# Kernel optimization log

Measured on AMD Instinct MI355X. Metric: run time of the kernel, lower is better.

Reference implementation:

```python
import jax, jax.numpy as jnp
import numpy as np

B, T, I, H, O = 1024, 512, 128, 256, 64


def setup_inputs() -> dict:
    key = jax.random.key(0)
    ks = jax.random.split(key, 12)
    def lin(k, shape, fan_in):
        return jax.random.uniform(k, shape, jnp.float32, -1.0, 1.0) / np.sqrt(fan_in)
    return {
        "x": jax.random.normal(ks[0], (B, T, I), jnp.float32),
        "h0": jnp.zeros((B, H), jnp.float32),
        # GRUCell params (gate order: r, z, n as in PyTorch)
        "W_ih": lin(ks[1], (3 * H, I), H),
        "b_ih": lin(ks[2], (3 * H,), H),
        "W_hh": lin(ks[3], (3 * H, H), H),
        "b_hh": lin(ks[4], (3 * H,), H),
        # input_transform Linear(I -> H)
        "Wt": lin(ks[5], (H, I), I),
        "bt": lin(ks[6], (H,), I),
        # output_proj Linear(H -> O)
        "Wo": lin(ks[7], (O, H), H),
        "bo": lin(ks[8], (O,), H),
        # gate_proj Linear(H -> O)
        "Wg": lin(ks[9], (O, H), H),
        "bg": lin(ks[10], (O,), H),
    }


def reference(x, h0, W_ih, b_ih, W_hh, b_hh, Wt, bt, Wo, bo, Wg, bg):
    # Precompute all input-side projections with big GEMMs (time-major for scan)
    xi = jnp.einsum("bti,gi->tbg", x, W_ih) + b_ih          # [T,B,3H]
    ti = jax.nn.silu(jnp.einsum("bti,hi->tbh", x, Wt) + bt)  # [T,B,H]

    def step(h, inp):
        xi_t, ti_t = inp
        hh = h @ W_hh.T + b_hh                               # [B,3H]
        xr, xz, xn = jnp.split(xi_t, 3, axis=-1)
        hr, hz, hn = jnp.split(hh, 3, axis=-1)
        r = jax.nn.sigmoid(xr + hr)
        z = jax.nn.sigmoid(xz + hz)
        n = jnp.tanh(xn + r * hn)
        h_new = (1.0 - z) * n + z * h
        proj = (h_new + ti_t) @ Wo.T + bo                    # [B,O]
        gate = jax.nn.sigmoid(h_new @ Wg.T + bg)             # [B,O]
        return h_new, proj * gate

    _, outs = jax.lax.scan(step, h0, (xi, ti))               # outs: [T,B,O]
    return jnp.mean(outs, axis=0)                            # [B,O]
```

## Files before the change

kernel.cpp:

```cpp
#include <hip/hip_runtime.h>
#include <hip/hip_bf16.h>


typedef __attribute__((ext_vector_type(8))) __bf16 bf16x8;
typedef __attribute__((ext_vector_type(4))) __bf16 bf16x4;
typedef __attribute__((ext_vector_type(4))) float f32x4;

#define MFMA(a, b, c) __builtin_amdgcn_mfma_f32_16x16x32_bf16(a, b, c, 0, 0, 0)

__device__ __forceinline__ float fsig(float v) {
  float e = __builtin_amdgcn_exp2f(v * -1.442695041f);
  return __builtin_amdgcn_rcpf(1.0f + e);
}
__device__ __forceinline__ float ftanh(float v) {
  float e = __builtin_amdgcn_exp2f(v * 2.885390082f);
  return 1.0f - 2.0f * __builtin_amdgcn_rcpf(1.0f + e);
}

#define O_WIN 0u
#define O_WHH 262144u
#define O_WO  655360u
#define O_WG  688128u
#define O_B1  720896u
#define O_H   724992u
#define O_ACC 1773568u
#define O_TIO 2035712u

__global__ void k1_prep(const float* __restrict__ Wih, const float* __restrict__ Wt,
                        const float* __restrict__ Whh, const float* __restrict__ Wo,
                        const float* __restrict__ Wg, const float* __restrict__ bih,
                        const float* __restrict__ bhh, const float* __restrict__ bt,
                        const float* __restrict__ h0, char* __restrict__ ws) {
  unsigned n = blockIdx.x * 256u + threadIdx.x;
  __bf16* win = (__bf16*)(ws + O_WIN);
  __bf16* whh = (__bf16*)(ws + O_WHH);
  __bf16* wo = (__bf16*)(ws + O_WO);
  __bf16* wg = (__bf16*)(ws + O_WG);
  float* b1 = (float*)(ws + O_B1);
  float* hb = (float*)(ws + O_H);
  float* ac = (float*)(ws + O_ACC);
  if (n < 98304u) win[n] = (__bf16)Wih[n];
  else if (n < 131072u) { unsigned i = n - 98304u; win[98304u + i] = (__bf16)Wt[i]; }
  else if (n < 327680u) { unsigned i = n - 131072u; whh[i] = (__bf16)Whh[i]; }
  else if (n < 344064u) { unsigned i = n - 327680u; wo[i] = (__bf16)Wo[i]; }
  else if (n < 360448u) { unsigned i = n - 344064u; wg[i] = (__bf16)Wg[i]; }
  else if (n < 361472u) {
    unsigned i = n - 360448u;
    float v = (i < 512u) ? (bih[i] + bhh[i]) : ((i < 768u) ? bih[i] : bt[i - 768u]);
    b1[i] = v;
  } else if (n < 623616u) { unsigned i = n - 361472u; hb[i] = h0[i]; }
  else if (n < 689152u) { unsigned i = n - 623616u; ac[i] = 0.0f; }
}

__global__ __launch_bounds__(256, 2) void k2_xi(
    const float* __restrict__ x, const __bf16* __restrict__ win,
    const float* __restrict__ b1, __bf16* __restrict__ xi, int t0, int tcbits) {
  extern __shared__ char sm2[];
  __bf16* Asm = (__bf16*)sm2;
  __bf16* Bsm = (__bf16*)(sm2 + 34816);
  const int tid = threadIdx.x;
  const int lane = tid & 63, wv = tid >> 6;
  const int m0 = blockIdx.x * 128;
  const int tcm = (1 << tcbits) - 1;
#pragma unroll
  for (int rnd = 0; rnd < 16; ++rnd) {
    int row = rnd * 8 + (tid >> 5);
    int cr = m0 + row;
    int bb = cr >> tcbits, tt = cr & tcm;
    const float* xr = x + ((size_t)bb * 512 + (size_t)(t0 + tt)) * 128 + (tid & 31) * 4;
    float4 v = *(const float4*)xr;
    bf16x4 b4 = {(__bf16)v.x, (__bf16)v.y, (__bf16)v.z, (__bf16)v.w};
    *(bf16x4*)&Asm[row * 136 + (tid & 31) * 4] = b4;
  }
  for (int nc = 0; nc < 6; ++nc) {
    __syncthreads();
#pragma unroll
    for (int rnd = 0; rnd < 8; ++rnd) {
      int rr = rnd * 16 + (tid >> 4);
      uint4 w4 = *(const uint4*)(win + (size_t)(nc * 128 + rr) * 128 + (tid & 15) * 8);
      *(uint4*)&Bsm[rr * 136 + (tid & 15) * 8] = w4;
    }
    __syncthreads();
    f32x4 zv = {0.f, 0.f, 0.f, 0.f};
    f32x4 acc[2][8];
#pragma unroll
    for (int mi = 0; mi < 2; ++mi)
#pragma unroll
      for (int nt = 0; nt < 8; ++nt) acc[mi][nt] = zv;
#pragma unroll
    for (int kt = 0; kt < 4; ++kt) {
      bf16x8 a0 = *(const bf16x8*)&Asm[(wv * 32 + (lane & 15)) * 136 + kt * 32 + (lane >> 4) * 8];
      bf16x8 a1 = *(const bf16x8*)&Asm[(wv * 32 + 16 + (lane & 15)) * 136 + kt * 32 + (lane >> 4) * 8];
#pragma unroll
      for (int nt = 0; nt < 8; ++nt) {
        bf16x8 b = *(const bf16x8*)&Bsm[(nt * 16 + (lane & 15)) * 136 + kt * 32 + (lane >> 4) * 8];
        acc[0][nt] = MFMA(a0, b, acc[0][nt]);
        acc[1][nt] = MFMA(a1, b, acc[1][nt]);
      }
    }
    __syncthreads();
#pragma unroll
    for (int nt = 0; nt < 8; ++nt) {
      float bv = b1[nc * 128 + nt * 16 + (lane & 15)];
#pragma unroll
      for (int mi = 0; mi < 2; ++mi)
#pragma unroll
        for (int r = 0; r < 4; ++r) {
          int rowb = wv * 32 + mi * 16 + (lane >> 4) * 4 + r;
          Bsm[rowb * 136 + nt * 16 + (lane & 15)] = (__bf16)(acc[mi][nt][r] + bv);
        }
    }
    __syncthreads();
#pragma unroll
    for (int rnd = 0; rnd < 8; ++rnd) {
      int row = rnd * 16 + (tid >> 4);
      int cr = m0 + row;
      int bb = cr >> tcbits, tt = cr & tcm;
      uint4 v = *(const uint4*)&Bsm[row * 136 + (tid & 15) * 8];
      *(uint4*)(xi + ((size_t)tt * 1024 + bb) * 768 + nc * 128 + (tid & 15) * 8) = v;
    }
  }
}

__global__ __launch_bounds__(256, 1) void k2_tio(
    const float* __restrict__ x, const __bf16* __restrict__ win,
    const __bf16* __restrict__ wo, const float* __restrict__ b1,
    const float* __restrict__ bo, __bf16* __restrict__ tio, int t0, int tcbits) {
  extern __shared__ char sm3[];
  __bf16* Asm = (__bf16*)sm3;
  __bf16* Bsm = (__bf16*)(sm3 + 34816);
  __bf16* Ti = (__bf16*)(sm3 + 69632);
  const int tid = threadIdx.x;
  const int lane = tid & 63, wv = tid >> 6;
  const int m0 = blockIdx.x * 128;
  const int tcm = (1 << tcbits) - 1;
#pragma unroll
  for (int rnd = 0; rnd < 16; ++rnd) {
    int row = rnd * 8 + (tid >> 5);
    int cr = m0 + row;
    int bb = cr >> tcbits, tt = cr & tcm;
    const float* xr = x + ((size_t)bb * 512 + (size_t)(t0 + tt)) * 128 + (tid & 31) * 4;
    float4 v = *(const float4*)xr;
    bf16x4 b4 = {(__bf16)v.x, (__bf16)v.y, (__bf16)v.z, (__bf16)v.w};
    *(bf16x4*)&Asm[row * 136 + (tid & 31) * 4] = b4;
  }
  for (int nc = 0; nc < 2; ++nc) {
    __syncthreads();
#pragma unroll
    for (int rnd = 0; rnd < 8; ++rnd) {
      int rr = rnd * 16 + (tid >> 4);
      uint4 w4 = *(const uint4*)(win + (size_t)(98304 / 128 + nc * 128 + rr) * 128 + (tid & 15) * 8);
      *(uint4*)&Bsm[rr * 136 + (tid & 15) * 8] = w4;
    }
    __syncthreads();
    f32x4 zv = {0.f, 0.f, 0.f, 0.f};
    f32x4 acc[2][8];
#pragma unroll
    for (int mi = 0; mi < 2; ++mi)
#pragma unroll
      for (int nt = 0; nt < 8; ++nt) acc[mi][nt] = zv;
#pragma unroll
    for (int kt = 0; kt < 4; ++kt) {
      bf16x8 a0 = *(const bf16x8*)&Asm[(wv * 32 + (lane & 15)) * 136 + kt * 32 + (lane >> 4) * 8];
      bf16x8 a1 = *(const bf16x8*)&Asm[(wv * 32 + 16 + (lane & 15)) * 136 + kt * 32 + (lane >> 4) * 8];
#pragma unroll
      for (int nt = 0; nt < 8; ++nt) {
        bf16x8 b = *(const bf16x8*)&Bsm[(nt * 16 + (lane & 15)) * 136 + kt * 32 + (lane >> 4) * 8];
        acc[0][nt] = MFMA(a0, b, acc[0][nt]);
        acc[1][nt] = MFMA(a1, b, acc[1][nt]);
      }
    }
#pragma unroll
    for (int nt = 0; nt < 8; ++nt) {
      float bv = b1[768 + nc * 128 + nt * 16 + (lane & 15)];
#pragma unroll
      for (int mi = 0; mi < 2; ++mi)
#pragma unroll
        for (int r = 0; r < 4; ++r) {
          int rowb = wv * 32 + mi * 16 + (lane >> 4) * 4 + r;
          float s = acc[mi][nt][r] + bv;
          s = s * __builtin_amdgcn_rcpf(1.0f + __builtin_amdgcn_exp2f(s * -1.442695041f));
          Ti[rowb * 264 + nc * 128 + nt * 16 + (lane & 15)] = (__bf16)s;
        }
    }
  }
  __syncthreads();
  for (int i = tid; i < 2048; i += 256) {
    int row = i >> 5;
    int c8 = (i & 31) * 8;
    *(uint4*)&Bsm[row * 264 + c8] = *(const uint4*)(wo + row * 256 + c8);
  }
  __syncthreads();
  f32x4 zv = {0.f, 0.f, 0.f, 0.f};
  f32x4 acc2[2][4];
#pragma unroll
  for (int mi = 0; mi < 2; ++mi)
#pragma unroll
    for (int nt = 0; nt < 4; ++nt) acc2[mi][nt] = zv;
#pragma unroll
  for (int kt = 0; kt < 8; ++kt) {
    bf16x8 a0 = *(const bf16x8*)&Ti[(wv * 32 + (lane & 15)) * 264 + kt * 32 + (lane >> 4) * 8];
    bf16x8 a1 = *(const bf16x8*)&Ti[(wv * 32 + 16 + (lane & 15)) * 264 + kt * 32 + (lane >> 4) * 8];
#pragma unroll
    for (int nt = 0; nt < 4; ++nt) {
      bf16x8 b = *(const bf16x8*)&Bsm[(nt * 16 + (lane & 15)) * 264 + kt * 32 + (lane >> 4) * 8];
      acc2[0][nt] = MFMA(a0, b, acc2[0][nt]);
      acc2[1][nt] = MFMA(a1, b, acc2[1][nt]);
    }
  }
#pragma unroll
  for (int nt = 0; nt < 4; ++nt) {
    int col = nt * 16 + (lane & 15);
    float bv = bo[col];
#pragma unroll
    for (int mi = 0; mi < 2; ++mi)
#pragma unroll
      for (int r = 0; r < 4; ++r) {
        int rowb = wv * 32 + mi * 16 + (lane >> 4) * 4 + r;
        int cr = m0 + rowb;
        int bb = cr >> tcbits, tt = cr & tcm;
        tio[((size_t)tt * 1024 + bb) * 64 + col] = (__bf16)(acc2[mi][nt][r] + bv);
      }
  }
}

__global__ __launch_bounds__(256, 1) void k3_rec(
    const __bf16* __restrict__ xi, const __bf16* __restrict__ tio,
    const __bf16* __restrict__ whh, const __bf16* __restrict__ wo,
    const __bf16* __restrict__ wg, const float* __restrict__ bhn,
    const float* __restrict__ bg, float* __restrict__ hbuf,
    float* __restrict__ accb, int TC) {
  extern __shared__ char sm[];
  __bf16* h_lds = (__bf16*)sm;
  float* pre = (float*)(sm + 8448);
  __bf16* xib = (__bf16*)(sm + 20736);
  __bf16* wow = (__bf16*)(sm + 34048);
  const int tid = threadIdx.x;
  const int lane = tid & 63, wv = tid >> 6;
  const int b0 = blockIdx.x * 4;
  const int gcp = lane * 4;

  bf16x8 wf[4][3][8];
#pragma unroll
  for (int p = 0; p < 4; ++p)
#pragma unroll
    for (int g = 0; g < 3; ++g)
#pragma unroll
      for (int kt = 0; kt < 8; ++kt) {
        int rowg = g * 256 + wv * 64 + p * 16 + (lane & 15);
        wf[p][g][kt] = *(const bf16x8*)(whh + (size_t)rowg * 256 + kt * 32 + (lane >> 4) * 8);
      }
  for (int i = tid; i < 4096; i += 256) {
    int row = i >> 5;
    int c8 = (i & 31) * 8;
    const __bf16* srcw = (row < 64) ? (wo + row * 256 + c8) : (wg + (row - 64) * 256 + c8);
    *(uint4*)&wow[row * 264 + c8] = *(const uint4*)srcw;
  }
  for (int i = tid; i < 2112; i += 256) ((unsigned*)h_lds)[i] = 0u;
  __syncthreads();
  float hreg[4];
  {
    f32x4 h4 = *(const f32x4*)(hbuf + (size_t)(b0 + wv) * 256 + gcp);
    hreg[0] = h4[0]; hreg[1] = h4[1]; hreg[2] = h4[2]; hreg[3] = h4[3];
    bf16x4 hb = {(__bf16)h4[0], (__bf16)h4[1], (__bf16)h4[2], (__bf16)h4[3]};
    *(bf16x4*)&h_lds[wv * 264 + gcp] = hb;
  }
  float bhnp[4];
#pragma unroll
  for (int p = 0; p < 4; ++p) bhnp[p] = bhn[wv * 64 + p * 16 + (lane & 15)];
  float bgv = bg[wv * 16 + (lane & 15)];
  float oacc[4] = {0.f, 0.f, 0.f, 0.f};
  if (lane < 16) {
#pragma unroll
    for (int r = 0; r < 4; ++r) oacc[r] = accb[(size_t)(b0 + r) * 64 + wv * 16 + lane];
  }
  {
    const uint2* s0 = (const uint2*)(xi + (size_t)b0 * 768);
    uint2* d0 = (uint2*)xib;
    d0[tid] = s0[tid]; d0[tid + 256] = s0[tid + 256]; d0[tid + 512] = s0[tid + 512];
    if (tid < 64) ((uint2*)(xib + 3072))[tid] = ((const uint2*)(tio + (size_t)b0 * 64))[tid];
  }
  __syncthreads();

#pragma unroll 1
  for (int t = 0; t < TC; ++t) {
    const int cur = t & 1, nxt = cur ^ 1;
    __bf16* xc = xib + cur * 3328;
    __bf16* xnb = xib + nxt * 3328;
    int tn = (t + 1 < TC) ? (t + 1) : t;
    uint2 pf0, pf1, pf2, pft;
    {
      const uint2* s = (const uint2*)(xi + ((size_t)tn * 1024 + b0) * 768);
      pf0 = s[tid]; pf1 = s[tid + 256]; pf2 = s[tid + 512];
      if (tid < 64) pft = ((const uint2*)(tio + ((size_t)tn * 1024 + b0) * 64))[tid];
    }
    bf16x8 afr[8];
#pragma unroll
    for (int kt = 0; kt < 8; ++kt)
      afr[kt] = *(const bf16x8*)&h_lds[(lane & 15) * 264 + kt * 32 + (lane >> 4) * 8];
#pragma unroll
    for (int p = 0; p < 4; ++p) {
      f32x4 ar = {0.f, 0.f, 0.f, 0.f}, az = {0.f, 0.f, 0.f, 0.f};
      f32x4 an = {bhnp[p], bhnp[p], bhnp[p], bhnp[p]};
#pragma unroll
      for (int kt = 0; kt < 8; ++kt) {
        ar = MFMA(afr[kt], wf[p][0][kt], ar);
        az = MFMA(afr[kt], wf[p][1][kt], az);
        an = MFMA(afr[kt], wf[p][2][kt], an);
      }
      if (lane < 16) {
        int col = wv * 64 + p * 16 + lane;
#pragma unroll
        for (int r = 0; r < 4; ++r) {
          pre[r * 256 + col] = ar[r];
          pre[1024 + r * 256 + col] = az[r];
          pre[2048 + r * 256 + col] = an[r];
        }
      }
    }
    __syncthreads();
    {
      f32x4 hr = *(const f32x4*)&pre[wv * 256 + gcp];
      f32x4 hz = *(const f32x4*)&pre[1024 + wv * 256 + gcp];
      f32x4 hn = *(const f32x4*)&pre[2048 + wv * 256 + gcp];
      bf16x4 xr4 = *(const bf16x4*)&xc[wv * 768 + gcp];
      bf16x4 xz4 = *(const bf16x4*)&xc[wv * 768 + 256 + gcp];
      bf16x4 xn4 = *(const bf16x4*)&xc[wv * 768 + 512 + gcp];
#pragma unroll
      for (int j = 0; j < 4; ++j) {
        float r = fsig((float)xr4[j] + hr[j]);
        float z = fsig((float)xz4[j] + hz[j]);
        float n = ftanh((float)xn4[j] + r * hn[j]);
        hreg[j] = n + z * (hreg[j] - n);
      }
      bf16x4 hb = {(__bf16)hreg[0], (__bf16)hreg[1], (__bf16)hreg[2], (__bf16)hreg[3]};
      *(bf16x4*)&h_lds[wv * 264 + gcp] = hb;
    }
    {
      uint2* d = (uint2*)xnb;
      d[tid] = pf0; d[tid + 256] = pf1; d[tid + 512] = pf2;
      if (tid < 64) ((uint2*)(xnb + 3072))[tid] = pft;
    }
    __syncthreads();
    {
      bf16x8 af2[8];
#pragma unroll
      for (int kt = 0; kt < 8; ++kt)
        af2[kt] = *(const bf16x8*)&h_lds[(lane & 15) * 264 + kt * 32 + (lane >> 4) * 8];
      f32x4 po = {0.f, 0.f, 0.f, 0.f};
      f32x4 pg = {bgv, bgv, bgv, bgv};
#pragma unroll
      for (int kt = 0; kt < 8; ++kt) {
        bf16x8 bfo = *(const bf16x8*)&wow[(wv * 16 + (lane & 15)) * 264 + kt * 32 + (lane >> 4) * 8];
        bf16x8 bfg = *(const bf16x8*)&wow[(64 + wv * 16 + (lane & 15)) * 264 + kt * 32 + (lane >> 4) * 8];
        po = MFMA(af2[kt], bfo, po);
        pg = MFMA(af2[kt], bfg, pg);
      }
      if (lane < 16) {
#pragma unroll
        for (int r = 0; r < 4; ++r) {
          float tv = (float)xc[3072 + r * 64 + wv * 16 + lane];
          float pov = po[r] + tv;
          float gv = fsig(pg[r]);
          oacc[r] += pov * gv;
        }
      }
    }
  }
  {
    f32x4 h4 = {hreg[0], hreg[1], hreg[2], hreg[3]};
    *(f32x4*)(hbuf + (size_t)(b0 + wv) * 256 + gcp) = h4;
  }
  if (lane < 16) {
#pragma unroll
    for (int r = 0; r < 4; ++r) accb[(size_t)(b0 + r) * 64 + wv * 16 + lane] = oacc[r];
  }
}

__global__ void k4_out(const float* __restrict__ accb, float* __restrict__ out) {
  int i = blockIdx.x * 256 + threadIdx.x;
  out[i] = accb[i] * (1.0f / 512.0f);
}

extern "C" void kernel_launch(void* const* d_in, const int* in_sizes, int n_in,
                              void* d_out, int out_size, void* d_ws, size_t ws_size,
                              hipStream_t stream) {
  const float* x = (const float*)d_in[0];
  const float* h0 = (const float*)d_in[1];
  const float* Wih = (const float*)d_in[2];
  const float* bih = (const float*)d_in[3];
  const float* Whh = (const float*)d_in[4];
  const float* bhh = (const float*)d_in[5];
  const float* Wt = (const float*)d_in[6];
  const float* bt = (const float*)d_in[7];
  const float* Wo = (const float*)d_in[8];
  const float* bo = (const float*)d_in[9];
  const float* Wg = (const float*)d_in[10];
  const float* bg = (const float*)d_in[11];
  float* out = (float*)d_out;
  char* ws = (char*)d_ws;

  int TC = 512;
  while (TC > 1 && (2035712ull + (size_t)TC * 1703936ull) > ws_size) TC >>= 1;
  int tcbits = 0;
  while ((1 << tcbits) != TC) ++tcbits;

  __bf16* win = (__bf16*)(ws + O_WIN);
  __bf16* whhb = (__bf16*)(ws + O_WHH);
  __bf16* wob = (__bf16*)(ws + O_WO);
  __bf16* wgb = (__bf16*)(ws + O_WG);
  float* b1 = (float*)(ws + O_B1);
  float* hbuf = (float*)(ws + O_H);
  float* accb = (float*)(ws + O_ACC);
  __bf16* tioc = (__bf16*)(ws + O_TIO);
  __bf16* xic = (__bf16*)(ws + O_TIO + (size_t)TC * 131072u);

  (void)hipFuncSetAttribute((const void*)k2_xi, hipFuncAttributeMaxDynamicSharedMemorySize, 69632);
  (void)hipFuncSetAttribute((const void*)k2_tio, hipFuncAttributeMaxDynamicSharedMemorySize, 137216);
  (void)hipFuncSetAttribute((const void*)k3_rec, hipFuncAttributeMaxDynamicSharedMemorySize, 101632);

  k1_prep<<<2692, 256, 0, stream>>>(Wih, Wt, Whh, Wo, Wg, bih, bhh, bt, h0, ws);
  int nch = 512 / TC;
  for (int c = 0; c < nch; ++c) {
    int t0 = c * TC;
    k2_xi<<<8 * TC, 256, 69632, stream>>>(x, win, b1, xic, t0, tcbits);
    k2_tio<<<8 * TC, 256, 137216, stream>>>(x, win, wob, b1, bo, tioc, t0, tcbits);
    k3_rec<<<256, 256, 101632, stream>>>(xic, tioc, whhb, wob, wgb, bhh + 512, bg, hbuf, accb, TC);
  }
  k4_out<<<256, 256, 0, stream>>>(accb, out);
}
```

Baseline: 2.223 ms.

## Restructure GRU recurrence to 8 waves with one barrier per step

Doubles the recurrent kernel's block to 512 threads so each wave owns half as many W_hh gate columns held in registers. The Wo and Wg weights also move from LDS into registers, split across wave halves. The hidden state is double-buffered and each wave keeps its own gate pre-activation scratch, which cuts the per-step barriers from two to one. The output/gate projection is computed from the previous step's h alongside the gate MFMAs and its result is applied one step late, so it is taken off the serial dependency chain. The cost is pipeline bookkeeping and an epilogue, and a wave that is idle or lightly loaded on the output work.

```diff
diff --git a/kernel.cpp b/kernel.cpp
--- a/kernel.cpp
+++ b/kernel.cpp
@@ -4,7 +4,9 @@
 
 typedef __attribute__((ext_vector_type(8))) __bf16 bf16x8;
 typedef __attribute__((ext_vector_type(4))) __bf16 bf16x4;
+typedef __attribute__((ext_vector_type(2))) __bf16 bf16x2;
 typedef __attribute__((ext_vector_type(4))) float f32x4;
+typedef __attribute__((ext_vector_type(2))) float f32x2;
 
 #define MFMA(a, b, c) __builtin_amdgcn_mfma_f32_16x16x32_bf16(a, b, c, 0, 0, 0)
 
@@ -224,82 +226,101 @@
   }
 }
 
-__global__ __launch_bounds__(256, 1) void k3_rec(
+__global__ __launch_bounds__(512, 1) void k3_rec(
     const __bf16* __restrict__ xi, const __bf16* __restrict__ tio,
     const __bf16* __restrict__ whh, const __bf16* __restrict__ wo,
     const __bf16* __restrict__ wg, const float* __restrict__ bhn,
     const float* __restrict__ bg, float* __restrict__ hbuf,
     float* __restrict__ accb, int TC) {
   extern __shared__ char sm[];
-  __bf16* h_lds = (__bf16*)sm;
-  float* pre = (float*)(sm + 8448);
-  __bf16* xib = (__bf16*)(sm + 20736);
-  __bf16* wow = (__bf16*)(sm + 34048);
+  __bf16* hbase = (__bf16*)sm;
+  float* preb = (float*)(sm + 16896);
+  __bf16* xib = (__bf16*)(sm + 30720);
+  float* pjb = (float*)(sm + 44032);
   const int tid = threadIdx.x;
   const int lane = tid & 63, wv = tid >> 6;
   const int b0 = blockIdx.x * 4;
-  const int gcp = lane * 4;
-
-  bf16x8 wf[4][3][8];
-#pragma unroll
-  for (int p = 0; p < 4; ++p)
+  const int l15 = lane & 15, lg = lane >> 4;
+  float* pre_w = preb + wv * 432;
+
+  bf16x8 wf[2][3][8];
+#pragma unroll
+  for (int p = 0; p < 2; ++p)
 #pragma unroll
     for (int g = 0; g < 3; ++g)
 #pragma unroll
       for (int kt = 0; kt < 8; ++kt) {
-        int rowg = g * 256 + wv * 64 + p * 16 + (lane & 15);
-        wf[p][g][kt] = *(const bf16x8*)(whh + (size_t)rowg * 256 + kt * 32 + (lane >> 4) * 8);
-      }
-  for (int i = tid; i < 4096; i += 256) {
-    int row = i >> 5;
-    int c8 = (i & 31) * 8;
-    const __bf16* srcw = (row < 64) ? (wo + row * 256 + c8) : (wg + (row - 64) * 256 + c8);
-    *(uint4*)&wow[row * 264 + c8] = *(const uint4*)srcw;
-  }
-  for (int i = tid; i < 2112; i += 256) ((unsigned*)h_lds)[i] = 0u;
+        int rowg = g * 256 + wv * 32 + p * 16 + l15;
+        wf[p][g][kt] = *(const bf16x8*)(whh + (size_t)rowg * 256 + kt * 32 + lg * 8);
+      }
+  const __bf16* wsrc = (wv < 4) ? (wo + (size_t)(wv * 16 + l15) * 256)
+                                : (wg + (size_t)((wv - 4) * 16 + l15) * 256);
+  bf16x8 wpf[8];
+#pragma unroll
+  for (int kt = 0; kt < 8; ++kt) wpf[kt] = *(const bf16x8*)(wsrc + kt * 32 + lg * 8);
+
+  float bhnp[2];
+#pragma unroll
+  for (int p = 0; p < 2; ++p) bhnp[p] = bhn[wv * 32 + p * 16 + l15];
+  const float bgv = (wv >= 4) ? bg[(wv - 4) * 16 + l15] : 0.0f;
+
+  for (int i = tid; i < 4224; i += 512) ((unsigned*)sm)[i] = 0u;
   __syncthreads();
-  float hreg[4];
+  const int row = lg;
+  const int c2 = l15 * 2;
+  float hreg[2];
   {
-    f32x4 h4 = *(const f32x4*)(hbuf + (size_t)(b0 + wv) * 256 + gcp);
-    hreg[0] = h4[0]; hreg[1] = h4[1]; hreg[2] = h4[2]; hreg[3] = h4[3];
-    bf16x4 hb = {(__bf16)h4[0], (__bf16)h4[1], (__bf16)h4[2], (__bf16)h4[3]};
-    *(bf16x4*)&h_lds[wv * 264 + gcp] = hb;
-  }
-  float bhnp[4];
-#pragma unroll
-  for (int p = 0; p < 4; ++p) bhnp[p] = bhn[wv * 64 + p * 16 + (lane & 15)];
-  float bgv = bg[wv * 16 + (lane & 15)];
+    const float* hp = hbuf + (size_t)(b0 + row) * 256 + wv * 32 + c2;
+    hreg[0] = hp[0];
+    hreg[1] = hp[1];
+    bf16x2 h2 = {(__bf16)hreg[0], (__bf16)hreg[1]};
+    *(bf16x2*)&hbase[row * 264 + wv * 32 + c2] = h2;
+  }
   float oacc[4] = {0.f, 0.f, 0.f, 0.f};
-  if (lane < 16) {
+  if (wv < 4 && lane < 16) {
 #pragma unroll
     for (int r = 0; r < 4; ++r) oacc[r] = accb[(size_t)(b0 + r) * 64 + wv * 16 + lane];
   }
   {
-    const uint2* s0 = (const uint2*)(xi + (size_t)b0 * 768);
-    uint2* d0 = (uint2*)xib;
-    d0[tid] = s0[tid]; d0[tid + 256] = s0[tid + 256]; d0[tid + 512] = s0[tid + 512];
-    if (tid < 64) ((uint2*)(xib + 3072))[tid] = ((const uint2*)(tio + (size_t)b0 * 64))[tid];
-  }
+    const uint2* s = (const uint2*)(xi + (size_t)b0 * 768);
+    uint2* d = (uint2*)xib;
+    d[tid] = s[tid];
+    if (tid < 256) d[512 + tid] = s[512 + tid];
+    if (tid < 64) d[768 + tid] = ((const uint2*)(tio + (size_t)b0 * 64))[tid];
+  }
+  float tioA[4] = {0.f, 0.f, 0.f, 0.f}, tioB[4] = {0.f, 0.f, 0.f, 0.f};
+  f32x4 poA = {0.f, 0.f, 0.f, 0.f};
   __syncthreads();
 
 #pragma unroll 1
   for (int t = 0; t < TC; ++t) {
     const int cur = t & 1, nxt = cur ^ 1;
-    __bf16* xc = xib + cur * 3328;
-    __bf16* xnb = xib + nxt * 3328;
+    const __bf16* hcur = hbase + cur * 4224;
+    __bf16* hnxt = hbase + nxt * 4224;
+    const __bf16* xc = xib + cur * 3328;
     int tn = (t + 1 < TC) ? (t + 1) : t;
-    uint2 pf0, pf1, pf2, pft;
+    uint2 pf0, pf1, pft;
     {
       const uint2* s = (const uint2*)(xi + ((size_t)tn * 1024 + b0) * 768);
-      pf0 = s[tid]; pf1 = s[tid + 256]; pf2 = s[tid + 512];
+      pf0 = s[tid];
+      if (tid < 256) pf1 = s[512 + tid];
       if (tid < 64) pft = ((const uint2*)(tio + ((size_t)tn * 1024 + b0) * 64))[tid];
     }
     bf16x8 afr[8];
 #pragma unroll
     for (int kt = 0; kt < 8; ++kt)
-      afr[kt] = *(const bf16x8*)&h_lds[(lane & 15) * 264 + kt * 32 + (lane >> 4) * 8];
-#pragma unroll
-    for (int p = 0; p < 4; ++p) {
+      afr[kt] = *(const bf16x8*)&hcur[l15 * 264 + kt * 32 + lg * 8];
+    if (t >= 2 && wv < 4 && lane < 16) {
+      const float* pj = pjb + ((t - 1) & 1) * 256;
+#pragma unroll
+      for (int r = 0; r < 4; ++r)
+        oacc[r] += (poA[r] + tioA[r]) * fsig(pj[r * 64 + wv * 16 + lane]);
+    }
+    f32x4 pN = {bgv, bgv, bgv, bgv};
+#pragma unroll
+    for (int kt = 0; kt < 8; ++kt) pN = MFMA(afr[kt], wpf[kt], pN);
+#pragma unroll
+    for (int p = 0; p < 2; ++p) {
       f32x4 ar = {0.f, 0.f, 0.f, 0.f}, az = {0.f, 0.f, 0.f, 0.f};
       f32x4 an = {bhnp[p], bhnp[p], bhnp[p], bhnp[p]};
 #pragma unroll
@@ -309,69 +330,86 @@
         an = MFMA(afr[kt], wf[p][2][kt], an);
       }
       if (lane < 16) {
-        int col = wv * 64 + p * 16 + lane;
 #pragma unroll
         for (int r = 0; r < 4; ++r) {
-          pre[r * 256 + col] = ar[r];
-          pre[1024 + r * 256 + col] = az[r];
-          pre[2048 + r * 256 + col] = an[r];
+          pre_w[(0 + r) * 36 + p * 16 + lane] = ar[r];
+          pre_w[(4 + r) * 36 + p * 16 + lane] = az[r];
+          pre_w[(8 + r) * 36 + p * 16 + lane] = an[r];
         }
       }
     }
-    __syncthreads();
     {
-      f32x4 hr = *(const f32x4*)&pre[wv * 256 + gcp];
-      f32x4 hz = *(const f32x4*)&pre[1024 + wv * 256 + gcp];
-      f32x4 hn = *(const f32x4*)&pre[2048 + wv * 256 + gcp];
-      bf16x4 xr4 = *(const bf16x4*)&xc[wv * 768 + gcp];
-      bf16x4 xz4 = *(const bf16x4*)&xc[wv * 768 + 256 + gcp];
-      bf16x4 xn4 = *(const bf16x4*)&xc[wv * 768 + 512 + gcp];
-#pragma unroll
-      for (int j = 0; j < 4; ++j) {
-        float r = fsig((float)xr4[j] + hr[j]);
-        float z = fsig((float)xz4[j] + hz[j]);
-        float n = ftanh((float)xn4[j] + r * hn[j]);
-        hreg[j] = n + z * (hreg[j] - n);
-      }
-      bf16x4 hb = {(__bf16)hreg[0], (__bf16)hreg[1], (__bf16)hreg[2], (__bf16)hreg[3]};
-      *(bf16x4*)&h_lds[wv * 264 + gcp] = hb;
-    }
+      f32x2 hr = *(const f32x2*)&pre_w[(0 + row) * 36 + c2];
+      f32x2 hz = *(const f32x2*)&pre_w[(4 + row) * 36 + c2];
+      f32x2 hn = *(const f32x2*)&pre_w[(8 + row) * 36 + c2];
+      bf16x2 xr2 = *(const bf16x2*)&xc[row * 768 + wv * 32 + c2];
+      bf16x2 xz2 = *(const bf16x2*)&xc[row * 768 + 256 + wv * 32 + c2];
+      bf16x2 xn2 = *(const bf16x2*)&xc[row * 768 + 512 + wv * 32 + c2];
+#pragma unroll
+      for (int j = 0; j < 2; ++j) {
+        float r_ = fsig((float)xr2[j] + hr[j]);
+        float z_ = fsig((float)xz2[j] + hz[j]);
+        float n_ = ftanh((float)xn2[j] + r_ * hn[j]);
+        hreg[j] = n_ + z_ * (hreg[j] - n_);
+      }
+      bf16x2 h2 = {(__bf16)hreg[0], (__bf16)hreg[1]};
+      *(bf16x2*)&hnxt[row * 264 + wv * 32 + c2] = h2;
+    }
+    if (wv >= 4 && lane < 16) {
+      float* pj = pjb + cur * 256;
+#pragma unroll
+      for (int r = 0; r < 4; ++r) pj[r * 64 + (wv - 4) * 16 + lane] = pN[r];
+    }
+    if (wv < 4 && lane < 16) {
+#pragma unroll
+      for (int r = 0; r < 4; ++r) {
+        tioA[r] = tioB[r];
+        tioB[r] = (float)xc[3072 + r * 64 + wv * 16 + lane];
+      }
+    }
+    poA = pN;
     {
-      uint2* d = (uint2*)xnb;
-      d[tid] = pf0; d[tid + 256] = pf1; d[tid + 512] = pf2;
-      if (tid < 64) ((uint2*)(xnb + 3072))[tid] = pft;
-    }
-    __syncthreads();
-    {
-      bf16x8 af2[8];
-#pragma unroll
-      for (int kt = 0; kt < 8; ++kt)
-        af2[kt] = *(const bf16x8*)&h_lds[(lane & 15) * 264 + kt * 32 + (lane >> 4) * 8];
-      f32x4 po = {0.f, 0.f, 0.f, 0.f};
-      f32x4 pg = {bgv, bgv, bgv, bgv};
-#pragma unroll
-      for (int kt = 0; kt < 8; ++kt) {
-        bf16x8 bfo = *(const bf16x8*)&wow[(wv * 16 + (lane & 15)) * 264 + kt * 32 + (lane >> 4) * 8];
-        bf16x8 bfg = *(const bf16x8*)&wow[(64 + wv * 16 + (lane & 15)) * 264 + kt * 32 + (lane >> 4) * 8];
-        po = MFMA(af2[kt], bfo, po);
-        pg = MFMA(af2[kt], bfg, pg);
-      }
-      if (lane < 16) {
-#pragma unroll
-        for (int r = 0; r < 4; ++r) {
-          float tv = (float)xc[3072 + r * 64 + wv * 16 + lane];
-          float pov = po[r] + tv;
-          float gv = fsig(pg[r]);
-          oacc[r] += pov * gv;
-        }
-      }
-    }
+      uint2* d = (uint2*)(xib + nxt * 3328);
+      d[tid] = pf0;
+      if (tid < 256) d[512 + tid] = pf1;
+      if (tid < 64) d[768 + tid] = pft;
+    }
+    __syncthreads();
+  }
+  if (TC >= 2 && wv < 4 && lane < 16) {
+    const float* pj = pjb + ((TC - 1) & 1) * 256;
+#pragma unroll
+    for (int r = 0; r < 4; ++r)
+      oacc[r] += (poA[r] + tioA[r]) * fsig(pj[r * 64 + wv * 16 + lane]);
   }
   {
-    f32x4 h4 = {hreg[0], hreg[1], hreg[2], hreg[3]};
-    *(f32x4*)(hbuf + (size_t)(b0 + wv) * 256 + gcp) = h4;
-  }
-  if (lane < 16) {
+    const __bf16* hcur = hbase + (TC & 1) * 4224;
+    bf16x8 af[8];
+#pragma unroll
+    for (int kt = 0; kt < 8; ++kt)
+      af[kt] = *(const bf16x8*)&hcur[l15 * 264 + kt * 32 + lg * 8];
+    f32x4 pN = {bgv, bgv, bgv, bgv};
+#pragma unroll
+    for (int kt = 0; kt < 8; ++kt) pN = MFMA(af[kt], wpf[kt], pN);
+    if (wv >= 4 && lane < 16) {
+      float* pj = pjb + (TC & 1) * 256;
+#pragma unroll
+      for (int r = 0; r < 4; ++r) pj[r * 64 + (wv - 4) * 16 + lane] = pN[r];
+    }
+    __syncthreads();
+    if (wv < 4 && lane < 16) {
+      const float* pj = pjb + (TC & 1) * 256;
+#pragma unroll
+      for (int r = 0; r < 4; ++r)
+        oacc[r] += (pN[r] + tioB[r]) * fsig(pj[r * 64 + wv * 16 + lane]);
+    }
+  }
+  {
+    float* hp = hbuf + (size_t)(b0 + row) * 256 + wv * 32 + c2;
+    hp[0] = hreg[0];
+    hp[1] = hreg[1];
+  }
+  if (wv < 4 && lane < 16) {
 #pragma unroll
     for (int r = 0; r < 4; ++r) accb[(size_t)(b0 + r) * 64 + wv * 16 + lane] = oacc[r];
   }
@@ -417,7 +455,7 @@
 
   (void)hipFuncSetAttribute((const void*)k2_xi, hipFuncAttributeMaxDynamicSharedMemorySize, 69632);
   (void)hipFuncSetAttribute((const void*)k2_tio, hipFuncAttributeMaxDynamicSharedMemorySize, 137216);
-  (void)hipFuncSetAttribute((const void*)k3_rec, hipFuncAttributeMaxDynamicSharedMemorySize, 101632);
+  (void)hipFuncSetAttribute((const void*)k3_rec, hipFuncAttributeMaxDynamicSharedMemorySize, 46080);
 
   k1_prep<<<2692, 256, 0, stream>>>(Wih, Wt, Whh, Wo, Wg, bih, bhh, bt, h0, ws);
   int nch = 512 / TC;
@@ -425,7 +463,7 @@
     int t0 = c * TC;
     k2_xi<<<8 * TC, 256, 69632, stream>>>(x, win, b1, xic, t0, tcbits);
     k2_tio<<<8 * TC, 256, 137216, stream>>>(x, win, wob, b1, bo, tioc, t0, tcbits);
-    k3_rec<<<256, 256, 101632, stream>>>(xic, tioc, whhb, wob, wgb, bhh + 512, bg, hbuf, accb, TC);
+    k3_rec<<<256, 512, 46080, stream>>>(xic, tioc, whhb, wob, wgb, bhh + 512, bg, hbuf, accb, TC);
   }
   k4_out<<<256, 256, 0, stream>>>(accb, out);
 }
```

After: 4.159 ms. +87.1%, slower.

## Remap GRU gate ownership per wave and defer output projection to cut barriers

Applied to the files above, without the earlier changes.

Each wave now applies the gate nonlinearities to the same hidden columns it computed in its MFMA, using a per-wave scratch area. This removes the block-wide barrier between the recurrent matmul and the gate update. The hidden state is double-buffered in LDS, and the output/gate projection for step t-1 is computed in step t from the already-loaded h fragments, with a tail step after the loop. Together these cut the per-step barriers from two to one and drop a second set of LDS fragment reads, at the cost of more shared memory and slightly more complex bookkeeping of the delayed output term.

```diff
diff --git a/kernel.cpp b/kernel.cpp
--- a/kernel.cpp
+++ b/kernel.cpp
@@ -4,6 +4,7 @@
 
 typedef __attribute__((ext_vector_type(8))) __bf16 bf16x8;
 typedef __attribute__((ext_vector_type(4))) __bf16 bf16x4;
+typedef __attribute__((ext_vector_type(2))) __bf16 bf16x2;
 typedef __attribute__((ext_vector_type(4))) float f32x4;
 
 #define MFMA(a, b, c) __builtin_amdgcn_mfma_f32_16x16x32_bf16(a, b, c, 0, 0, 0)
@@ -231,14 +232,15 @@
     const float* __restrict__ bg, float* __restrict__ hbuf,
     float* __restrict__ accb, int TC) {
   extern __shared__ char sm[];
-  __bf16* h_lds = (__bf16*)sm;
-  float* pre = (float*)(sm + 8448);
-  __bf16* xib = (__bf16*)(sm + 20736);
-  __bf16* wow = (__bf16*)(sm + 34048);
+  __bf16* hbase = (__bf16*)sm;
+  float* preb = (float*)(sm + 16896);
+  __bf16* xib = (__bf16*)(sm + 29952);
+  __bf16* wow = (__bf16*)(sm + 43264);
   const int tid = threadIdx.x;
   const int lane = tid & 63, wv = tid >> 6;
   const int b0 = blockIdx.x * 4;
-  const int gcp = lane * 4;
+  const int l15 = lane & 15, lg = lane >> 4;
+  float* pre_w = preb + wv * 816;
 
   bf16x8 wf[4][3][8];
 #pragma unroll
@@ -247,8 +249,8 @@
     for (int g = 0; g < 3; ++g)
 #pragma unroll
       for (int kt = 0; kt < 8; ++kt) {
-        int rowg = g * 256 + wv * 64 + p * 16 + (lane & 15);
-        wf[p][g][kt] = *(const bf16x8*)(whh + (size_t)rowg * 256 + kt * 32 + (lane >> 4) * 8);
+        int rowg = g * 256 + wv * 64 + p * 16 + l15;
+        wf[p][g][kt] = *(const bf16x8*)(whh + (size_t)rowg * 256 + kt * 32 + lg * 8);
       }
   for (int i = tid; i < 4096; i += 256) {
     int row = i >> 5;
@@ -256,19 +258,21 @@
     const __bf16* srcw = (row < 64) ? (wo + row * 256 + c8) : (wg + (row - 64) * 256 + c8);
     *(uint4*)&wow[row * 264 + c8] = *(const uint4*)srcw;
   }
-  for (int i = tid; i < 2112; i += 256) ((unsigned*)h_lds)[i] = 0u;
+  for (int i = tid; i < 4224; i += 256) ((unsigned*)sm)[i] = 0u;
   __syncthreads();
+  const int row = lg;
+  const int c4 = l15 * 4;
   float hreg[4];
   {
-    f32x4 h4 = *(const f32x4*)(hbuf + (size_t)(b0 + wv) * 256 + gcp);
+    f32x4 h4 = *(const f32x4*)(hbuf + (size_t)(b0 + row) * 256 + wv * 64 + c4);
     hreg[0] = h4[0]; hreg[1] = h4[1]; hreg[2] = h4[2]; hreg[3] = h4[3];
     bf16x4 hb = {(__bf16)h4[0], (__bf16)h4[1], (__bf16)h4[2], (__bf16)h4[3]};
-    *(bf16x4*)&h_lds[wv * 264 + gcp] = hb;
+    *(bf16x4*)&hbase[row * 264 + wv * 64 + c4] = hb;
   }
   float bhnp[4];
 #pragma unroll
-  for (int p = 0; p < 4; ++p) bhnp[p] = bhn[wv * 64 + p * 16 + (lane & 15)];
-  float bgv = bg[wv * 16 + (lane & 15)];
+  for (int p = 0; p < 4; ++p) bhnp[p] = bhn[wv * 64 + p * 16 + l15];
+  const float bgv = bg[wv * 16 + l15];
   float oacc[4] = {0.f, 0.f, 0.f, 0.f};
   if (lane < 16) {
 #pragma unroll
@@ -280,13 +284,15 @@
     d0[tid] = s0[tid]; d0[tid + 256] = s0[tid + 256]; d0[tid + 512] = s0[tid + 512];
     if (tid < 64) ((uint2*)(xib + 3072))[tid] = ((const uint2*)(tio + (size_t)b0 * 64))[tid];
   }
+  float tioR[4] = {0.f, 0.f, 0.f, 0.f};
   __syncthreads();
 
 #pragma unroll 1
   for (int t = 0; t < TC; ++t) {
     const int cur = t & 1, nxt = cur ^ 1;
-    __bf16* xc = xib + cur * 3328;
-    __bf16* xnb = xib + nxt * 3328;
+    const __bf16* hcur = hbase + cur * 4224;
+    __bf16* hnxt = hbase + nxt * 4224;
+    const __bf16* xc = xib + cur * 3328;
     int tn = (t + 1 < TC) ? (t + 1) : t;
     uint2 pf0, pf1, pf2, pft;
     {
@@ -297,7 +303,7 @@
     bf16x8 afr[8];
 #pragma unroll
     for (int kt = 0; kt < 8; ++kt)
-      afr[kt] = *(const bf16x8*)&h_lds[(lane & 15) * 264 + kt * 32 + (lane >> 4) * 8];
+      afr[kt] = *(const bf16x8*)&hcur[l15 * 264 + kt * 32 + lg * 8];
 #pragma unroll
     for (int p = 0; p < 4; ++p) {
       f32x4 ar = {0.f, 0.f, 0.f, 0.f}, az = {0.f, 0.f, 0.f, 0.f};
@@ -309,67 +315,82 @@
         an = MFMA(afr[kt], wf[p][2][kt], an);
       }
       if (lane < 16) {
-        int col = wv * 64 + p * 16 + lane;
 #pragma unroll
         for (int r = 0; r < 4; ++r) {
-          pre[r * 256 + col] = ar[r];
-          pre[1024 + r * 256 + col] = az[r];
-          pre[2048 + r * 256 + col] = an[r];
+          pre_w[r * 68 + p * 16 + lane] = ar[r];
+          pre_w[272 + r * 68 + p * 16 + lane] = az[r];
+          pre_w[544 + r * 68 + p * 16 + lane] = an[r];
         }
       }
     }
-    __syncthreads();
     {
-      f32x4 hr = *(const f32x4*)&pre[wv * 256 + gcp];
-      f32x4 hz = *(const f32x4*)&pre[1024 + wv * 256 + gcp];
-      f32x4 hn = *(const f32x4*)&pre[2048 + wv * 256 + gcp];
-      bf16x4 xr4 = *(const bf16x4*)&xc[wv * 768 + gcp];
-      bf16x4 xz4 = *(const bf16x4*)&xc[wv * 768 + 256 + gcp];
-      bf16x4 xn4 = *(const bf16x4*)&xc[wv * 768 + 512 + gcp];
+      f32x4 hr = *(const f32x4*)&pre_w[row * 68 + c4];
+      f32x4 hz = *(const f32x4*)&pre_w[272 + row * 68 + c4];
+      f32x4 hn = *(const f32x4*)&pre_w[544 + row * 68 + c4];
+      bf16x4 xr4 = *(const bf16x4*)&xc[row * 768 + wv * 64 + c4];
+      bf16x4 xz4 = *(const bf16x4*)&xc[row * 768 + 256 + wv * 64 + c4];
+      bf16x4 xn4 = *(const bf16x4*)&xc[row * 768 + 512 + wv * 64 + c4];
 #pragma unroll
       for (int j = 0; j < 4; ++j) {
-        float r = fsig((float)xr4[j] + hr[j]);
-        float z = fsig((float)xz4[j] + hz[j]);
-        float n = ftanh((float)xn4[j] + r * hn[j]);
-        hreg[j] = n + z * (hreg[j] - n);
+        float r_ = fsig((float)xr4[j] + hr[j]);
+        float z_ = fsig((float)xz4[j] + hz[j]);
+        float n_ = ftanh((float)xn4[j] + r_ * hn[j]);
+        hreg[j] = n_ + z_ * (hreg[j] - n_);
       }
       bf16x4 hb = {(__bf16)hreg[0], (__bf16)hreg[1], (__bf16)hreg[2], (__bf16)hreg[3]};
-      *(bf16x4*)&h_lds[wv * 264 + gcp] = hb;
+      *(bf16x4*)&hnxt[row * 264 + wv * 64 + c4] = hb;
     }
     {
-      uint2* d = (uint2*)xnb;
-      d[tid] = pf0; d[tid + 256] = pf1; d[tid + 512] = pf2;
-      if (tid < 64) ((uint2*)(xnb + 3072))[tid] = pft;
-    }
-    __syncthreads();
-    {
-      bf16x8 af2[8];
-#pragma unroll
-      for (int kt = 0; kt < 8; ++kt)
-        af2[kt] = *(const bf16x8*)&h_lds[(lane & 15) * 264 + kt * 32 + (lane >> 4) * 8];
       f32x4 po = {0.f, 0.f, 0.f, 0.f};
       f32x4 pg = {bgv, bgv, bgv, bgv};
 #pragma unroll
       for (int kt = 0; kt < 8; ++kt) {
-        bf16x8 bfo = *(const bf16x8*)&wow[(wv * 16 + (lane & 15)) * 264 + kt * 32 + (lane >> 4) * 8];
-        bf16x8 bfg = *(const bf16x8*)&wow[(64 + wv * 16 + (lane & 15)) * 264 + kt * 32 + (lane >> 4) * 8];
-        po = MFMA(af2[kt], bfo, po);
-        pg = MFMA(af2[kt], bfg, pg);
-      }
-      if (lane < 16) {
-#pragma unroll
-        for (int r = 0; r < 4; ++r) {
-          float tv = (float)xc[3072 + r * 64 + wv * 16 + lane];
-          float pov = po[r] + tv;
-          float gv = fsig(pg[r]);
-          oacc[r] += pov * gv;
-        }
-      }
+        bf16x8 bfo = *(const bf16x8*)&wow[(wv * 16 + l15) * 264 + kt * 32 + lg * 8];
+        bf16x8 bfg = *(const bf16x8*)&wow[(64 + wv * 16 + l15) * 264 + kt * 32 + lg * 8];
+        po = MFMA(afr[kt], bfo, po);
+        pg = MFMA(afr[kt], bfg, pg);
+      }
+      if (t >= 1 && lane < 16) {
+#pragma unroll
+        for (int r = 0; r < 4; ++r)
+          oacc[r] += (po[r] + tioR[r]) * fsig(pg[r]);
+      }
+    }
+    if (lane < 16) {
+#pragma unroll
+      for (int r = 0; r < 4; ++r) tioR[r] = (float)xc[3072 + r * 64 + wv * 16 + lane];
+    }
+    {
+      uint2* d = (uint2*)(xib + nxt * 3328);
+      d[tid] = pf0; d[tid + 256] = pf1; d[tid + 512] = pf2;
+      if (tid < 64) ((uint2*)(xib + nxt * 3328 + 3072))[tid] = pft;
+    }
+    __syncthreads();
+  }
+  {
+    const __bf16* hcur = hbase + (TC & 1) * 4224;
+    bf16x8 af[8];
+#pragma unroll
+    for (int kt = 0; kt < 8; ++kt)
+      af[kt] = *(const bf16x8*)&hcur[l15 * 264 + kt * 32 + lg * 8];
+    f32x4 po = {0.f, 0.f, 0.f, 0.f};
+    f32x4 pg = {bgv, bgv, bgv, bgv};
+#pragma unroll
+    for (int kt = 0; kt < 8; ++kt) {
+      bf16x8 bfo = *(const bf16x8*)&wow[(wv * 16 + l15) * 264 + kt * 32 + lg * 8];
+      bf16x8 bfg = *(const bf16x8*)&wow[(64 + wv * 16 + l15) * 264 + kt * 32 + lg * 8];
+      po = MFMA(af[kt], bfo, po);
+      pg = MFMA(af[kt], bfg, pg);
+    }
+    if (lane < 16) {
+#pragma unroll
+      for (int r = 0; r < 4; ++r)
+        oacc[r] += (po[r] + tioR[r]) * fsig(pg[r]);
     }
   }
   {
     f32x4 h4 = {hreg[0], hreg[1], hreg[2], hreg[3]};
-    *(f32x4*)(hbuf + (size_t)(b0 + wv) * 256 + gcp) = h4;
+    *(f32x4*)(hbuf + (size_t)(b0 + row) * 256 + wv * 64 + c4) = h4;
   }
   if (lane < 16) {
 #pragma unroll
@@ -417,7 +438,7 @@
 
   (void)hipFuncSetAttribute((const void*)k2_xi, hipFuncAttributeMaxDynamicSharedMemorySize, 69632);
   (void)hipFuncSetAttribute((const void*)k2_tio, hipFuncAttributeMaxDynamicSharedMemorySize, 137216);
-  (void)hipFuncSetAttribute((const void*)k3_rec, hipFuncAttributeMaxDynamicSharedMemorySize, 101632);
+  (void)hipFuncSetAttribute((const void*)k3_rec, hipFuncAttributeMaxDynamicSharedMemorySize, 110848);
 
   k1_prep<<<2692, 256, 0, stream>>>(Wih, Wt, Whh, Wo, Wg, bih, bhh, bt, h0, ws);
   int nch = 512 / TC;
@@ -425,7 +446,7 @@
     int t0 = c * TC;
     k2_xi<<<8 * TC, 256, 69632, stream>>>(x, win, b1, xic, t0, tcbits);
     k2_tio<<<8 * TC, 256, 137216, stream>>>(x, win, wob, b1, bo, tioc, t0, tcbits);
-    k3_rec<<<256, 256, 101632, stream>>>(xic, tioc, whhb, wob, wgb, bhh + 512, bg, hbuf, accb, TC);
+    k3_rec<<<256, 256, 110848, stream>>>(xic, tioc, whhb, wob, wgb, bhh + 512, bg, hbuf, accb, TC);
   }
   k4_out<<<256, 256, 0, stream>>>(accb, out);
 }
```

New measurement: 2.159 ms. 2.9% less time.
